# Kernel tuning notes

Hardware: AMD Instinct MI355X
Metric: run time of the kernel (lower is better)

## Reference

```python
import jax, jax.numpy as jnp
import numpy as np

B, LP, LQ, H = 16, 1024, 1024, 1024


def setup_inputs() -> dict:
    key = jax.random.key(0)
    k1, k2, k3 = jax.random.split(key, 3)
    p = jax.random.normal(k1, (B, LP, H), dtype=jnp.float32)
    q = jax.random.normal(k2, (B, LQ, H), dtype=jnp.float32)
    # Dense(hidden_size) kernel + bias (glorot-ish scale)
    W_key = jax.random.normal(k3, (H, H), dtype=jnp.float32) / np.sqrt(H)
    b_key = jnp.zeros((H,), dtype=jnp.float32)
    return {"p": p, "q": q, "W_key": W_key, "b_key": b_key}


def reference(p, q, W_key, b_key):
    # keys = Dense(q): [B, LQ, H]
    keys = jnp.einsum("bqh,hk->bqk", q, W_key) + b_key
    # attention scores p @ keys^T (no scaling): [B, LP, LQ]
    scores = jnp.einsum("bph,bqh->bpq", p, keys)
    attn = jax.nn.softmax(scores, axis=-1)
    # q reused as values; relu on output: [B, LP, H]
    out = jax.nn.relu(jnp.einsum("bpq,bqh->bph", attn, q))
    return out
```

## Files before the change

### kernel.cpp

```cpp
#include <hip/hip_runtime.h>
#include <hip/hip_bf16.h>

#define B_N 16
#define LP_N 1024
#define LQ_N 1024
#define H_N 1024

typedef unsigned short u16;
typedef __attribute__((ext_vector_type(8))) _Float16 f16x8;
typedef __attribute__((ext_vector_type(4))) float f32x4;

__device__ __forceinline__ u16 f2h(float x) {
    _Float16 h = (_Float16)x;
    return *(u16*)&h;
}
__device__ __forceinline__ float h2f(u16 u) {
    _Float16 h;
    *(u16*)&h = u;
    return (float)h;
}

__device__ __forceinline__ void load_lds16(const u16* g, u16* l) {
    __builtin_amdgcn_global_load_lds(
        (const __attribute__((address_space(1))) void*)g,
        (__attribute__((address_space(3))) void*)l, 16, 0, 0);
}

#define MFMA_F16(a, b, c) __builtin_amdgcn_mfma_f32_16x16x32_f16(a, b, c, 0, 0, 0)
#define VMW0()   asm volatile("s_waitcnt vmcnt(0)" ::: "memory")
#define LGKM12() asm volatile("s_waitcnt lgkmcnt(12)" ::: "memory")
#define LGKM8()  asm volatile("s_waitcnt lgkmcnt(8)" ::: "memory")
#define LGKM0()  asm volatile("s_waitcnt lgkmcnt(0)" ::: "memory")
#define SCHB()   __builtin_amdgcn_sched_barrier(0)
#define SBAR()   __builtin_amdgcn_s_barrier()

template<int BKT, bool SPLIT, int EPI>
__launch_bounds__(512, 2)
__global__ void gemm2t(const u16* __restrict__ Ahi, const u16* __restrict__ Alo,
                       const u16* __restrict__ Bm,
                       const float* __restrict__ bias,
                       float* __restrict__ Cf, u16* __restrict__ Ch,
                       int N, int gn, int gmn,
                       long long sA, long long sB, long long sC)
{
    constexpr int REG   = 256 * BKT;
    constexpr int O_AL  = REG;
    constexpr int O_B   = SPLIT ? 2 * REG : REG;
    constexpr int BUF   = O_B + REG;
    constexpr int NSUBK = BKT / 32;
    constexpr int CH    = BKT / 16;
    constexpr int RSTEP = 256 / CH;
    __shared__ __align__(16) u16 lds[2 * BUF];

    const int tid  = threadIdx.x;
    const int lane = tid & 63;
    const int wv   = tid >> 6;
    const int wr   = wv >> 2, wc = wv & 3;

    const int d   = blockIdx.x;
    const int cpx = gridDim.x >> 3;
    const int swz = (d & 7) * cpx + (d >> 3);
    const long long z = swz / gmn;
    const int r_  = swz % gmn;
    const int bm  = (r_ / gn) * 256;
    const int bn  = (r_ % gn) * 256;

    const char* pAh = (const char*)(Ahi + z * sA);
    const char* pAl = (const char*)(Alo + z * sA);
    const char* pB  = (const char*)(Bm + z * sB);

    const int rr  = (BKT == 32) ? (tid >> 2) : (tid >> 3);
    const int xcv = (BKT == 32) ? ((tid & 3) ^ ((rr >> 1) & 3))
                                : ((tid & 7) ^ (rr & 7));
    long long aofs[CH], bofs[CH];
#pragma unroll
    for (int j = 0; j < CH; ++j) {
        aofs[j] = (long long)(bm + rr + j * RSTEP) * 2048 + xcv * 16;
        bofs[j] = (long long)(bn + rr + j * RSTEP) * 2048 + xcv * 16;
    }

    int offA[8][NSUBK], offB[4][NSUBK];
#pragma unroll
    for (int i = 0; i < 8; ++i) {
        const int r = wr * 128 + i * 16 + (lane & 15);
#pragma unroll
        for (int s = 0; s < NSUBK; ++s) {
            if constexpr (BKT == 32)
                offA[i][s] = r * 32 + ((((lane >> 4) ^ (r >> 1)) & 3) << 3);
            else
                offA[i][s] = r * 64 + ((((s * 4 + (lane >> 4)) ^ r) & 7) << 3);
        }
    }
#pragma unroll
    for (int j = 0; j < 4; ++j) {
        const int r = wc * 64 + j * 16 + (lane & 15);
#pragma unroll
        for (int s = 0; s < NSUBK; ++s) {
            if constexpr (BKT == 32)
                offB[j][s] = r * 32 + ((((lane >> 4) ^ (r >> 1)) & 3) << 3);
            else
                offB[j][s] = r * 64 + ((((s * 4 + (lane >> 4)) ^ r) & 7) << 3);
        }
    }

    f32x4 acc[8][4];
#pragma unroll
    for (int i = 0; i < 8; ++i)
#pragma unroll
        for (int j = 0; j < 4; ++j)
            acc[i][j] = (f32x4){0.f, 0.f, 0.f, 0.f};

#define STG(NB, KB) do {                                                      \
        _Pragma("unroll")                                                     \
        for (int j = 0; j < CH; ++j) {                                        \
            load_lds16((const u16*)(pAh + aofs[j] + (KB)),                    \
                       lds + (NB) + tid * 8 + j * 4096);                      \
            load_lds16((const u16*)(pB + bofs[j] + (KB)),                     \
                       lds + (NB) + O_B + tid * 8 + j * 4096);                \
            if constexpr (SPLIT)                                              \
                load_lds16((const u16*)(pAl + aofs[j] + (KB)),                \
                           lds + (NB) + O_AL + tid * 8 + j * 4096);           \
        }                                                                     \
    } while (0)

#define TERM(AF, BF) do {                                                     \
        __builtin_amdgcn_s_setprio(1);                                        \
        _Pragma("unroll")                                                     \
        for (int i = 0; i < 8; ++i)                                           \
            _Pragma("unroll")                                                 \
            for (int j = 0; j < 4; ++j)                                       \
                acc[i][j] = MFMA_F16(AF[i], BF[j], acc[i][j]);                \
        __builtin_amdgcn_s_setprio(0);                                        \
    } while (0)

    constexpr int NT = 1024 / BKT;

    STG(0, 0);

    for (int t = 0; t < NT; ++t) {
        const int cb = (t & 1) ? BUF : 0;
        const int nb = (t & 1) ? 0 : BUF;
        const long long kb = (long long)(t + 1) * (BKT * 2);

        VMW0();
        SBAR();

        if constexpr (BKT == 32) {
            f16x8 b[4], ah[8], al[8];
#pragma unroll
            for (int j = 0; j < 4; ++j)
                b[j] = *(const f16x8*)(lds + cb + O_B + offB[j][0]);
#pragma unroll
            for (int i = 0; i < 8; ++i)
                ah[i] = *(const f16x8*)(lds + cb + offA[i][0]);
            if constexpr (SPLIT) {
#pragma unroll
                for (int i = 0; i < 8; ++i)
                    al[i] = *(const f16x8*)(lds + cb + O_AL + offA[i][0]);
            }
            if (t + 1 < NT) STG(nb, kb);
            if constexpr (SPLIT) { LGKM8(); } else { LGKM0(); }
            SCHB();
            TERM(ah, b);
            if constexpr (SPLIT) {
                LGKM0(); SCHB();
                TERM(al, b);
            }
        } else {
            f16x8 b0[4], a0[8], b1[4], a1[8];
#pragma unroll
            for (int j = 0; j < 4; ++j)
                b0[j] = *(const f16x8*)(lds + cb + O_B + offB[j][0]);
#pragma unroll
            for (int i = 0; i < 8; ++i)
                a0[i] = *(const f16x8*)(lds + cb + offA[i][0]);
            if (t + 1 < NT) STG(nb, kb);
#pragma unroll
            for (int j = 0; j < 4; ++j)
                b1[j] = *(const f16x8*)(lds + cb + O_B + offB[j][1]);
#pragma unroll
            for (int i = 0; i < 8; ++i)
                a1[i] = *(const f16x8*)(lds + cb + offA[i][1]);
            LGKM12(); SCHB();
            TERM(a0, b0);
            LGKM0(); SCHB();
            TERM(a1, b1);
        }
    }
#undef STG
#undef TERM

    const long long Cbase = z * sC;
#pragma unroll
    for (int i = 0; i < 8; ++i) {
        const int row0 = bm + wr * 128 + i * 16 + ((lane >> 4) << 2);
#pragma unroll
        for (int j = 0; j < 4; ++j) {
            const int col = bn + wc * 64 + j * 16 + (lane & 15);
#pragma unroll
            for (int e = 0; e < 4; ++e) {
                const float v = acc[i][j][e];
                const long long idx = Cbase + (long long)(row0 + e) * N + col;
                if constexpr (EPI == 0) {
                    Cf[idx] = v;
                } else if constexpr (EPI == 1) {
                    Ch[idx] = f2h(v + bias[col]);
                } else {
                    Cf[idx] = fmaxf(v, 0.f);
                }
            }
        }
    }
}

__global__ void cvt_f16(const float* __restrict__ in, u16* __restrict__ o16,
                        long long n4)
{
    const long long i = (long long)blockIdx.x * 256 + threadIdx.x;
    if (i >= n4) return;
    const float4 v = ((const float4*)in)[i];
    ushort4 h;
    h.x = f2h(v.x); h.y = f2h(v.y); h.z = f2h(v.z); h.w = f2h(v.w);
    ((ushort4*)o16)[i] = h;
}

__global__ void fuse_cvt_q(const float* __restrict__ q, u16* __restrict__ hi,
                           u16* __restrict__ lo, u16* __restrict__ thi)
{
    __shared__ float t[32][33];
    const long long z = blockIdx.z;
    const long long base = z * 1048576;
    const int r0 = blockIdx.y * 32, c0 = blockIdx.x * 32;
    for (int j = threadIdx.y; j < 32; j += 8) {
        const float v = q[base + (long long)(r0 + j) * 1024 + c0 + threadIdx.x];
        t[j][threadIdx.x] = v;
        const long long o = base + (long long)(r0 + j) * 1024 + c0 + threadIdx.x;
        const u16 h = f2h(v);
        hi[o] = h;
        lo[o] = f2h(v - h2f(h));
    }
    __syncthreads();
    for (int j = threadIdx.y; j < 32; j += 8)
        thi[base + (long long)(c0 + j) * 1024 + r0 + threadIdx.x] = f2h(t[threadIdx.x][j]);
}

__global__ void transpose_cvt_w(const float* __restrict__ in, u16* __restrict__ hi)
{
    __shared__ float t[32][33];
    const int r0 = blockIdx.y * 32, c0 = blockIdx.x * 32;
    for (int j = threadIdx.y; j < 32; j += 8)
        t[j][threadIdx.x] = in[(long long)(r0 + j) * 1024 + c0 + threadIdx.x];
    __syncthreads();
    for (int j = threadIdx.y; j < 32; j += 8)
        hi[(long long)(c0 + j) * 1024 + r0 + threadIdx.x] = f2h(t[threadIdx.x][j]);
}

__global__ void softmax_f16(const float* __restrict__ S, u16* __restrict__ A)
{
    const long long row = blockIdx.x;
    const float* r = S + row * (long long)LQ_N;
    const int t = threadIdx.x;
    float4 v = ((const float4*)r)[t];

    float m = fmaxf(fmaxf(v.x, v.y), fmaxf(v.z, v.w));
#pragma unroll
    for (int off = 32; off > 0; off >>= 1)
        m = fmaxf(m, __shfl_xor(m, off));

    __shared__ float red[4];
    const int lane = t & 63, wid = t >> 6;
    if (lane == 0) red[wid] = m;
    __syncthreads();
    m = fmaxf(fmaxf(red[0], red[1]), fmaxf(red[2], red[3]));
    __syncthreads();

    v.x = __expf(v.x - m); v.y = __expf(v.y - m);
    v.z = __expf(v.z - m); v.w = __expf(v.w - m);
    float s = v.x + v.y + v.z + v.w;
#pragma unroll
    for (int off = 32; off > 0; off >>= 1)
        s += __shfl_xor(s, off);
    if (lane == 0) red[wid] = s;
    __syncthreads();
    s = red[0] + red[1] + red[2] + red[3];

    const float inv = 1.0f / s;
    ushort4 o;
    o.x = f2h(v.x * inv); o.y = f2h(v.y * inv);
    o.z = f2h(v.z * inv); o.w = f2h(v.w * inv);
    ((ushort4*)(A + row * (long long)LQ_N))[t] = o;
}

#define BM 128
#define BN 128
#define BK 8
#define TM 8
#define TN 8

template<bool TRANSB, bool BIAS, bool RELU>
__launch_bounds__(256)
__global__ void gemm_k(const float* __restrict__ A, const float* __restrict__ Bmat,
                       const float* __restrict__ bias, float* __restrict__ C,
                       int M, int N, int K,
                       long long sA, long long sB, long long sC)
{
    __shared__ float As[BK][BM];
    __shared__ float Bs[BK][BN];
    const int tid = threadIdx.x;
    const int tx = tid & 15;
    const int ty = tid >> 4;
    const int bn = blockIdx.x * BN;
    const int bm = blockIdx.y * BM;
    const long long z = blockIdx.z;
    A += z * sA; Bmat += z * sB; C += z * sC;
    float acc[TM][TN];
#pragma unroll
    for (int i = 0; i < TM; i++)
#pragma unroll
        for (int j = 0; j < TN; j++) acc[i][j] = 0.f;
    const int arow = tid >> 1;
    const int acol = (tid & 1) * 4;
    const int bk_n = tid >> 5;
    const int bn_n = (tid & 31) * 4;
    for (int k0 = 0; k0 < K; k0 += BK) {
        float4 a4 = *(const float4*)&A[(long long)(bm + arow) * K + k0 + acol];
        As[acol + 0][arow] = a4.x; As[acol + 1][arow] = a4.y;
        As[acol + 2][arow] = a4.z; As[acol + 3][arow] = a4.w;
        if (TRANSB) {
            float4 b4 = *(const float4*)&Bmat[(long long)(bn + arow) * K + k0 + acol];
            Bs[acol + 0][arow] = b4.x; Bs[acol + 1][arow] = b4.y;
            Bs[acol + 2][arow] = b4.z; Bs[acol + 3][arow] = b4.w;
        } else {
            float4 b4 = *(const float4*)&Bmat[(long long)(k0 + bk_n) * N + bn + bn_n];
            *(float4*)&Bs[bk_n][bn_n] = b4;
        }
        __syncthreads();
#pragma unroll
        for (int k = 0; k < BK; k++) {
            float a[TM], b[TN];
            *(float4*)&a[0] = *(const float4*)&As[k][ty * TM];
            *(float4*)&a[4] = *(const float4*)&As[k][ty * TM + 4];
            *(float4*)&b[0] = *(const float4*)&Bs[k][tx * TN];
            *(float4*)&b[4] = *(const float4*)&Bs[k][tx * TN + 4];
#pragma unroll
            for (int i = 0; i < TM; i++)
#pragma unroll
                for (int j = 0; j < TN; j++)
                    acc[i][j] = fmaf(a[i], b[j], acc[i][j]);
        }
        __syncthreads();
    }
#pragma unroll
    for (int i = 0; i < TM; i++) {
        const int row = bm + ty * TM + i;
#pragma unroll
        for (int j = 0; j < TN; j += 4) {
            const int col = bn + tx * TN + j;
            float4 v;
            v.x = acc[i][j + 0]; v.y = acc[i][j + 1];
            v.z = acc[i][j + 2]; v.w = acc[i][j + 3];
            if (BIAS) {
                v.x += bias[col + 0]; v.y += bias[col + 1];
                v.z += bias[col + 2]; v.w += bias[col + 3];
            }
            if (RELU) {
                v.x = fmaxf(v.x, 0.f); v.y = fmaxf(v.y, 0.f);
                v.z = fmaxf(v.z, 0.f); v.w = fmaxf(v.w, 0.f);
            }
            *(float4*)&C[(long long)row * N + col] = v;
        }
    }
}

__global__ void softmax_k(float* __restrict__ S)
{
    const long long row = blockIdx.x;
    float* r = S + row * (long long)LQ_N;
    const int t = threadIdx.x;
    float4 v = ((float4*)r)[t];
    float m = fmaxf(fmaxf(v.x, v.y), fmaxf(v.z, v.w));
#pragma unroll
    for (int off = 32; off > 0; off >>= 1)
        m = fmaxf(m, __shfl_xor(m, off));
    __shared__ float red[4];
    const int lane = t & 63, wid = t >> 6;
    if (lane == 0) red[wid] = m;
    __syncthreads();
    m = fmaxf(fmaxf(red[0], red[1]), fmaxf(red[2], red[3]));
    __syncthreads();
    v.x = __expf(v.x - m); v.y = __expf(v.y - m);
    v.z = __expf(v.z - m); v.w = __expf(v.w - m);
    float s = v.x + v.y + v.z + v.w;
#pragma unroll
    for (int off = 32; off > 0; off >>= 1)
        s += __shfl_xor(s, off);
    if (lane == 0) red[wid] = s;
    __syncthreads();
    s = red[0] + red[1] + red[2] + red[3];
    const float inv = 1.0f / s;
    v.x *= inv; v.y *= inv; v.z *= inv; v.w *= inv;
    ((float4*)r)[t] = v;
}

extern "C" void kernel_launch(void* const* d_in, const int* in_sizes, int n_in,
                              void* d_out, int out_size, void* d_ws, size_t ws_size,
                              hipStream_t stream)
{
    const float* p    = (const float*)d_in[0];
    const float* q    = (const float*)d_in[1];
    const float* W    = (const float*)d_in[2];
    const float* bias = (const float*)d_in[3];
    float* out = (float*)d_out;

    const size_t MB32 = 33554432ull;
    const size_t NEED = 5 * MB32 + 2097152ull;

    if (ws_size >= NEED) {
        char* w = (char*)d_ws;
        u16* p16   = (u16*)(w + 0 * MB32);
        u16* q_hi  = (u16*)(w + 1 * MB32);
        u16* q_lo  = (u16*)(w + 2 * MB32);
        u16* keys  = (u16*)(w + 3 * MB32);
        u16* qT    = (u16*)(w + 4 * MB32);
        u16* Wt    = (u16*)(w + 5 * MB32);
        float* scores = (float*)(w + 1 * MB32);
        u16* attn     = (u16*)(w + 0 * MB32);

        const long long n4 = (long long)B_N * LQ_N * H_N / 4;
        cvt_f16<<<dim3((unsigned)(n4 / 256)), 256, 0, stream>>>(p, p16, n4);
        fuse_cvt_q<<<dim3(32, 32, B_N), dim3(32, 8), 0, stream>>>(q, q_hi, q_lo, qT);
        transpose_cvt_w<<<dim3(32, 32, 1), dim3(32, 8), 0, stream>>>(W, Wt);

        gemm2t<32, true, 1><<<256, 512, 0, stream>>>(
            q_hi, q_lo, Wt, bias, nullptr, keys,
            H_N, 4, 256, 0, 0, 0);

        gemm2t<64, false, 0><<<256, 512, 0, stream>>>(
            p16, p16, keys, nullptr, scores, nullptr,
            LQ_N, 4, 16,
            (long long)LP_N * H_N, (long long)LQ_N * H_N, (long long)LP_N * LQ_N);

        softmax_f16<<<B_N * LP_N, 256, 0, stream>>>(scores, attn);

        gemm2t<64, false, 2><<<256, 512, 0, stream>>>(
            attn, attn, qT, nullptr, out, nullptr,
            H_N, 4, 16,
            (long long)LP_N * LQ_N, (long long)H_N * LQ_N, (long long)LP_N * H_N);
    } else {
        float* keys   = (float*)d_ws;
        float* scores = keys + (long long)B_N * LQ_N * H_N;

        gemm_k<false, true, false><<<dim3(H_N / BN, (B_N * LQ_N) / BM, 1), 256, 0, stream>>>(
            q, W, bias, keys, B_N * LQ_N, H_N, H_N, 0, 0, 0);
        gemm_k<true, false, false><<<dim3(LQ_N / BN, LP_N / BM, B_N), 256, 0, stream>>>(
            p, keys, nullptr, scores, LP_N, LQ_N, H_N,
            (long long)LP_N * H_N, (long long)LQ_N * H_N, (long long)LP_N * LQ_N);
        softmax_k<<<B_N * LP_N, 256, 0, stream>>>(scores);
        gemm_k<false, false, true><<<dim3(H_N / BN, LP_N / BM, B_N), 256, 0, stream>>>(
            scores, q, nullptr, out, LP_N, H_N, LQ_N,
            (long long)LP_N * LQ_N, (long long)LQ_N * H_N, (long long)LP_N * H_N);
    }
}
```

Before: 227.6 us.

## Split-K the scores GEMM in two halves and sum partials inside softmax

The scores GEMM now launches 512 blocks, each covering half of the K=1024 reduction with BK=32, and writes two fp32 partial score buffers. The softmax kernel reads both partials and adds them before the max/exp/normalize. This doubles the block count to fill the device better (256 blocks on a large CU count with 2 blocks/CU occupancy) at the cost of an extra 64MB write and read of fp32 partials and a larger workspace requirement. The tile K step also shrinks from 64 to 32 for this GEMM.

```diff
diff --git a/kernel.cpp b/kernel.cpp
--- a/kernel.cpp
+++ b/kernel.cpp
@@ -34,14 +34,14 @@
 #define SCHB()   __builtin_amdgcn_sched_barrier(0)
 #define SBAR()   __builtin_amdgcn_s_barrier()
 
-template<int BKT, bool SPLIT, int EPI>
+template<int BKT, bool SPLIT, int EPI, bool SK>
 __launch_bounds__(512, 2)
 __global__ void gemm2t(const u16* __restrict__ Ahi, const u16* __restrict__ Alo,
                        const u16* __restrict__ Bm,
                        const float* __restrict__ bias,
                        float* __restrict__ Cf, u16* __restrict__ Ch,
                        int N, int gn, int gmn,
-                       long long sA, long long sB, long long sC)
+                       long long sA, long long sB, long long sC, long long sK)
 {
     constexpr int REG   = 256 * BKT;
     constexpr int O_AL  = REG;
@@ -60,14 +60,16 @@
     const int d   = blockIdx.x;
     const int cpx = gridDim.x >> 3;
     const int swz = (d & 7) * cpx + (d >> 3);
-    const long long z = swz / gmn;
-    const int r_  = swz % gmn;
+    int sw2 = swz, sk = 0;
+    if constexpr (SK) { sk = swz & 1; sw2 = swz >> 1; }
+    const long long z = sw2 / gmn;
+    const int r_  = sw2 % gmn;
     const int bm  = (r_ / gn) * 256;
     const int bn  = (r_ % gn) * 256;
 
-    const char* pAh = (const char*)(Ahi + z * sA);
-    const char* pAl = (const char*)(Alo + z * sA);
-    const char* pB  = (const char*)(Bm + z * sB);
+    const char* pAh = (const char*)(Ahi + z * sA) + sk * 1024;
+    const char* pAl = (const char*)(Alo + z * sA) + sk * 1024;
+    const char* pB  = (const char*)(Bm + z * sB) + sk * 1024;
 
     const int rr  = (BKT == 32) ? (tid >> 2) : (tid >> 3);
     const int xcv = (BKT == 32) ? ((tid & 3) ^ ((rr >> 1) & 3))
@@ -133,7 +135,7 @@
         __builtin_amdgcn_s_setprio(0);                                        \
     } while (0)
 
-    constexpr int NT = 1024 / BKT;
+    constexpr int NT = (SK ? 512 : 1024) / BKT;
 
     STG(0, 0);
 
@@ -190,7 +192,7 @@
 #undef STG
 #undef TERM
 
-    const long long Cbase = z * sC;
+    const long long Cbase = z * sC + (long long)sk * sK;
 #pragma unroll
     for (int i = 0; i < 8; ++i) {
         const int row0 = bm + wr * 128 + i * 16 + ((lane >> 4) << 2);
@@ -255,12 +257,17 @@
         hi[(long long)(c0 + j) * 1024 + r0 + threadIdx.x] = f2h(t[threadIdx.x][j]);
 }
 
-__global__ void softmax_f16(const float* __restrict__ S, u16* __restrict__ A)
+__global__ void softmax2_f16(const float* __restrict__ S0,
+                             const float* __restrict__ S1,
+                             u16* __restrict__ A)
 {
     const long long row = blockIdx.x;
-    const float* r = S + row * (long long)LQ_N;
     const int t = threadIdx.x;
-    float4 v = ((const float4*)r)[t];
+    const float4 u0 = ((const float4*)(S0 + row * (long long)LQ_N))[t];
+    const float4 u1 = ((const float4*)(S1 + row * (long long)LQ_N))[t];
+    float4 v;
+    v.x = u0.x + u1.x; v.y = u0.y + u1.y;
+    v.z = u0.z + u1.z; v.w = u0.w + u1.w;
 
     float m = fmaxf(fmaxf(v.x, v.y), fmaxf(v.z, v.w));
 #pragma unroll
@@ -413,7 +420,7 @@
     float* out = (float*)d_out;
 
     const size_t MB32 = 33554432ull;
-    const size_t NEED = 5 * MB32 + 2097152ull;
+    const size_t NEED = 5 * MB32 + 2097152ull + 2 * MB32;
 
     if (ws_size >= NEED) {
         char* w = (char*)d_ws;
@@ -423,29 +430,31 @@
         u16* keys  = (u16*)(w + 3 * MB32);
         u16* qT    = (u16*)(w + 4 * MB32);
         u16* Wt    = (u16*)(w + 5 * MB32);
-        float* scores = (float*)(w + 1 * MB32);
-        u16* attn     = (u16*)(w + 0 * MB32);
+        float* s0  = (float*)(w + 1 * MB32);
+        float* s1  = (float*)(w + 5 * MB32 + 2097152ull);
+        u16* attn  = (u16*)(w + 0 * MB32);
 
         const long long n4 = (long long)B_N * LQ_N * H_N / 4;
         cvt_f16<<<dim3((unsigned)(n4 / 256)), 256, 0, stream>>>(p, p16, n4);
         fuse_cvt_q<<<dim3(32, 32, B_N), dim3(32, 8), 0, stream>>>(q, q_hi, q_lo, qT);
         transpose_cvt_w<<<dim3(32, 32, 1), dim3(32, 8), 0, stream>>>(W, Wt);
 
-        gemm2t<32, true, 1><<<256, 512, 0, stream>>>(
+        gemm2t<32, true, 1, false><<<256, 512, 0, stream>>>(
             q_hi, q_lo, Wt, bias, nullptr, keys,
-            H_N, 4, 256, 0, 0, 0);
-
-        gemm2t<64, false, 0><<<256, 512, 0, stream>>>(
-            p16, p16, keys, nullptr, scores, nullptr,
+            H_N, 4, 256, 0, 0, 0, 0);
+
+        gemm2t<32, false, 0, true><<<512, 512, 0, stream>>>(
+            p16, p16, keys, nullptr, s0, nullptr,
             LQ_N, 4, 16,
-            (long long)LP_N * H_N, (long long)LQ_N * H_N, (long long)LP_N * LQ_N);
-
-        softmax_f16<<<B_N * LP_N, 256, 0, stream>>>(scores, attn);
-
-        gemm2t<64, false, 2><<<256, 512, 0, stream>>>(
+            (long long)LP_N * H_N, (long long)LQ_N * H_N, (long long)LP_N * LQ_N,
+            (long long)(s1 - s0));
+
+        softmax2_f16<<<B_N * LP_N, 256, 0, stream>>>(s0, s1, attn);
+
+        gemm2t<64, false, 2, false><<<256, 512, 0, stream>>>(
             attn, attn, qT, nullptr, out, nullptr,
             H_N, 4, 16,
-            (long long)LP_N * LQ_N, (long long)H_N * LQ_N, (long long)LP_N * H_N);
+            (long long)LP_N * LQ_N, (long long)H_N * LQ_N, (long long)LP_N * H_N, 0);
     } else {
         float* keys   = (float*)d_ws;
         float* scores = keys + (long long)B_N * LQ_N * H_N;
```

Result: slower. 251.2 us (+10.4%).
